# Kernel optimization log

Measured on AMD Instinct MI355X. Metric: run time of the kernel, lower is better.

Reference implementation:

```python
import jax, jax.numpy as jnp
import numpy as np

NUM_CLASSES = 20  # support_labels drawn from [0, 20); torch.unique over 200 samples yields all 20 w.h.p.


def setup_inputs() -> dict:
    key = jax.random.key(0)
    k1, k2, k3 = jax.random.split(key, 3)
    support_features = jax.random.normal(k1, (8, 200, 512), dtype=jnp.float32)
    support_labels = jax.random.randint(k2, (200,), 0, NUM_CLASSES, dtype=jnp.int64)
    query_features = jax.random.normal(k3, (8, 1024, 512), dtype=jnp.float32)
    return {
        "support_features": support_features,
        "support_labels": support_labels,
        "query_features": query_features,
    }


def _task_cov(x):
    # x: (P, T, F) -> per-phi covariance over the T samples, factor 1/(T-1)
    T = x.shape[1]
    xc = x - jnp.mean(x, axis=1, keepdims=True)
    return jnp.einsum("ptf,ptg->pfg", xc, xc) / (T - 1)


def reference(support_features, support_labels, query_features):
    P, T, F = support_features.shape
    C = NUM_CLASSES

    onehot = jax.nn.one_hot(support_labels, C, dtype=support_features.dtype)  # (T, C)
    counts = onehot.sum(axis=0)                                               # (C,)
    counts_safe = jnp.maximum(counts, 1.0)

    # per-class means: (P, C, F)
    class_means = jnp.einsum("ptf,tc->pcf", support_features, onehot) / counts_safe[None, :, None]

    # per-class covariance with 1/(n_c - 1) factor (matches _estimate_cov after transpose)
    centered = support_features[:, :, None, :] - class_means[:, None, :, :]   # (P, T, C, F)
    masked = centered * onehot[None, :, :, None]                               # zero out other classes
    denom = jnp.maximum(counts - 1.0, 1.0)
    class_cov = jnp.einsum("ptcf,ptcg->pcfg", masked, masked) / denom[None, :, None, None]

    task_cov = _task_cov(support_features)                                     # (P, F, F)

    lam = counts_safe / (counts_safe + 1.0)                                    # (C,)
    eye = jnp.eye(F, dtype=support_features.dtype)
    cov_reg = (lam[None, :, None, None] * class_cov
               + (1.0 - lam)[None, :, None, None] * task_cov[:, None]
               + eye)                                                          # (P, C, F, F)
    precision = jnp.linalg.inv(cov_reg)                                        # (P, C, F, F)

    # Mahalanobis quadratic form: diff^T P diff for every (phi, query, class)
    diff = class_means[:, None, :, :] - query_features[:, :, None, :]          # (P, Q, C, F)
    quad = jnp.einsum("pqcf,pcfg,pqcg->pqc", diff, precision, diff)
    mean_logits = (-quad).mean(axis=0)                                         # (Q, C)
    return mean_logits, class_means
```

## Files before the change

kernel.cpp:

```cpp
#include <hip/hip_runtime.h>

#define P 8
#define T 200
#define C 20
#define F 512
#define NQ 1024
#define MAXN 40
#define MMAX (T + MAXN)
#define PACK ((MMAX*(MMAX+1))/2)
#define PACKA 29280
#define PACKT 40960
#define QL (NQ*C)
#define NB 16
#define NTF 512
#define ETH 72
#define XQS 72

#define NBLK_FACTOR 160
#define NBLK_SQ     128
#define NBLK_MEANS  160
#define NBLK_QNORM  128
#define NBLK_TOTAL  (NBLK_FACTOR + NBLK_SQ + NBLK_MEANS + NBLK_QNORM)

enum : int {
  OFF_G    = 0,
  OFF_SQ   = OFF_G   + P*T*T,
  OFF_G1   = OFF_SQ  + P*T*NQ,
  OFF_GG   = OFF_G1  + P*T,
  OFF_GM   = OFF_GG  + P,
  OFF_GMC  = OFF_GM  + P*T*C,
  OFF_MM   = OFF_GMC + P*C,
  OFF_GQ   = OFF_MM  + P*C,
  OFF_QN   = OFF_GQ  + P*NQ,
  OFF_MQ   = OFF_QN  + P*NQ,
  OFF_W    = OFF_MQ  + P*C*NQ,
  OFF_QUAD = OFF_W   + P*C*PACKT,
  OFF_CLSF = OFF_QUAD+ P*NQ*C,
  OFF_INT  = OFF_CLSF+ C*8
};

typedef _Float16 f16x8 __attribute__((ext_vector_type(8)));
typedef _Float16 f16x4 __attribute__((ext_vector_type(4)));
typedef _Float16 f16x2 __attribute__((ext_vector_type(2)));
typedef float    f32x4 __attribute__((ext_vector_type(4)));

__device__ __forceinline__ int offr(int i){ return (i*(i+1))>>1; }

__device__ __forceinline__ int rowS(int i){
  int a = i >> 2, r = i & 3;
  return 8*a*(a+1) + 4*r*(a+1);
}

__device__ __forceinline__ int rowT(int r){
  const int R = r >> 6, s = r & 63;
  const int base = 4096 * ((R*(R+1)) >> 1);
  return base + s*((R+1) << 6);
}

__device__ __forceinline__ int row_of(int e){
  int i = (int)((sqrtf(8.f*(float)e + 1.f) - 1.f) * 0.5f);
  while (offr(i+1) <= e) ++i;
  while (offr(i) > e) --i;
  return i;
}

__device__ __forceinline__ int row_ofS(int e){
  int i = (int)sqrtf(2.f*(float)e);
  if (i > MMAX-1) i = MMAX-1;
  while (i < MMAX-1 && rowS(i+1) <= e) ++i;
  while (i > 0 && rowS(i) > e) --i;
  return i;
}

__global__ void k_setup(const int* lab, float* ws){
  int c = threadIdx.x;
  if (c >= C) return;
  int* wsI = (int*)(ws + OFF_INT);
  int n = 0;
  for (int t = 0; t < T; ++t){
    if (lab[t] == c){ if (n < MAXN) wsI[C + c*MAXN + n] = t; ++n; }
  }
  if (n > MAXN) n = MAXN;
  wsI[c] = n;
  float nf    = (float)n;
  float nsafe = fmaxf(nf, 1.0f);
  float dn    = fmaxf(nf - 1.0f, 1.0f);
  float lam   = nsafe / (nsafe + 1.0f);
  float sv    = (1.0f - lam) / (float)(T - 1);
  float av    = lam / dn;
  float* cf = ws + OFF_CLSF + c*8;
  cf[0] = nsafe; cf[1] = dn; cf[2] = lam; cf[3] = sv; cf[4] = av;
  cf[5] = sqrtf(sv); cf[6] = sqrtf(av); cf[7] = 0.0f;
}

__global__ __launch_bounds__(256) void k_gram(const float* X, float* ws){
  __shared__ float Xi[32][33];
  __shared__ float Xj[32][33];
  const int p = blockIdx.z, i0 = blockIdx.y*32, j0 = blockIdx.x*32;
  const int tx = threadIdx.x, ty = threadIdx.y;
  const int tid = ty*16 + tx;
  const float* Xp = X + (size_t)p*T*F;
  float acc[2][2] = {{0.f,0.f},{0.f,0.f}};
  for (int kb = 0; kb < F; kb += 32){
    for (int e = tid; e < 32*32; e += 256){
      int r = e >> 5, kk = e & 31;
      Xi[r][kk] = (i0+r < T) ? Xp[(i0+r)*F + kb+kk] : 0.f;
      Xj[r][kk] = (j0+r < T) ? Xp[(j0+r)*F + kb+kk] : 0.f;
    }
    __syncthreads();
    for (int kk = 0; kk < 32; ++kk){
      float a0 = Xi[2*ty][kk],   a1 = Xi[2*ty+1][kk];
      float b0 = Xj[2*tx][kk],   b1 = Xj[2*tx+1][kk];
      acc[0][0] += a0*b0; acc[0][1] += a0*b1;
      acc[1][0] += a1*b0; acc[1][1] += a1*b1;
    }
    __syncthreads();
  }
  float* Gp = ws + OFF_G + (size_t)p*T*T;
  for (int a = 0; a < 2; ++a)
    for (int b = 0; b < 2; ++b){
      int i = i0 + 2*ty + a, j = j0 + 2*tx + b;
      if (i < T && j < T) Gp[i*T + j] = acc[a][b];
    }
}

__global__ __launch_bounds__(256) void k_pstats_a(float* ws){
  const int p = blockIdx.y, bx = blockIdx.x;
  const int w = threadIdx.x >> 6, lane = threadIdx.x & 63;
  const int* wsI = (const int*)(ws + OFF_INT);
  const float* Gp = ws + OFF_G + (size_t)p*T*T;
  float* g1 = ws + OFF_G1 + p*T;
  float* Gm = ws + OFF_GM + (size_t)p*T*C;
  for (int rr = 0; rr < 2; ++rr){
    const int t = bx*8 + w*2 + rr;
    float s = 0.f;
    for (int u = lane; u < T; u += 64) s += Gp[t*T + u];
    for (int off = 32; off; off >>= 1) s += __shfl_down(s, off, 64);
    if (lane == 0) g1[t] = s * (1.0f/T);
    if (lane < C){
      int c = lane, nn = wsI[c];
      const int* idxc = wsI + C + c*MAXN;
      float sc = 0.f;
      for (int j = 0; j < nn; ++j) sc += Gp[t*T + idxc[j]];
      Gm[t*C + c] = sc / ws[OFF_CLSF + c*8];
    }
  }
}

__global__ __launch_bounds__(256) void k_pstats_b(float* ws){
  __shared__ float red[64];
  const int p = blockIdx.x, tid = threadIdx.x;
  const int* wsI = (const int*)(ws + OFF_INT);
  const float* g1 = ws + OFF_G1 + p*T;
  const float* Gm = ws + OFF_GM + (size_t)p*T*C;
  if (tid < 64){
    float s = 0.f;
    for (int t = tid; t < T; t += 64) s += g1[t];
    red[tid] = s;
  }
  __syncthreads();
  if (tid == 0){
    float s = 0.f;
    for (int k = 0; k < 64; ++k) s += red[k];
    ws[OFF_GG + p] = s * (1.0f/T);
  }
  if (tid < C){
    int c = tid, nn = wsI[c];
    const int* idxc = wsI + C + c*MAXN;
    float s = 0.f;
    for (int t = 0; t < T; ++t) s += Gm[t*C + c];
    ws[OFF_GMC + p*C + c] = s * (1.0f/T);
    float s2 = 0.f;
    for (int j = 0; j < nn; ++j) s2 += Gm[idxc[j]*C + c];
    ws[OFF_MM + p*C + c] = s2 / ws[OFF_CLSF + c*8];
  }
}

__global__ __launch_bounds__(256) void k_qstats(float* ws){
  __shared__ float red[4][64];
  const int p = blockIdx.y;
  const int qb = blockIdx.x*64;
  const int chunk = threadIdx.x >> 6, lane = threadIdx.x & 63;
  const int q = qb + lane;
  const int* wsI = (const int*)(ws + OFF_INT);
  const float* SQp = ws + OFF_SQ + (size_t)p*T*NQ;
  float s = 0.f;
  for (int t = chunk*50; t < chunk*50 + 50; ++t) s += SQp[t*NQ + q];
  red[chunk][lane] = s;
  __syncthreads();
  if (chunk == 0){
    float tot = red[0][lane] + red[1][lane] + red[2][lane] + red[3][lane];
    ws[OFF_GQ + p*NQ + q] = tot * (1.0f/T);
  }
  for (int c = chunk; c < C; c += 4){
    int nn = wsI[c];
    const int* idxc = wsI + C + c*MAXN;
    float sc = 0.f;
    for (int j = 0; j < nn; ++j) sc += SQp[idxc[j]*NQ + q];
    ws[OFF_MQ + ((size_t)(p*C + c))*NQ + q] = sc / ws[OFF_CLSF + c*8];
  }
}


union __align__(16) BigShared {
  struct { float Lp[PACKA]; float Sb[16*228]; float Dv[NB][NB+1]; } f;
  struct { _Float16 XHs[64*XQS], XLs[64*XQS], QHs[256*XQS], QLs[256*XQS]; } q;
};

__global__ __launch_bounds__(NTF) void k_big(const float* __restrict__ X,
                                             const float* __restrict__ Qf,
                                             float* __restrict__ ws,
                                             float* __restrict__ out){
  __shared__ BigShared u;
  const int bid = blockIdx.x;
  const int tid = threadIdx.x;
  const int* wsI = (const int*)(ws + OFF_INT);

  if (bid < NBLK_FACTOR){
    float* Lp = u.f.Lp;
    float* Sb = u.f.Sb;
    float (&Dv)[NB][NB+1] = u.f.Dv;
    const int blk = bid, p = blk / C, c = blk % C;
    const int n = wsI[c];
    const int m = T + n;
    const int* idxc = wsI + C + c*MAXN;
    const float* cf = ws + OFF_CLSF + c*8;
    const float sv = cf[3], av = cf[4], sqsa = cf[5]*cf[6];
    const float* Gp  = ws + OFF_G  + (size_t)p*T*T;
    const float* g1p = ws + OFF_G1 + p*T;
    const float  ggv = ws[OFF_GG + p];
    const float* Gmp = ws + OFF_GM + (size_t)p*T*C;
    const float gmcv = ws[OFF_GMC + p*C + c];
    const float mmv  = ws[OFF_MM  + p*C + c];

    for (int e = tid; e < PACKA; e += NTF){
      int i = row_ofS(e);
      int j = e - rowS(i);
      float v = 0.f;
      if (i < m && j <= i){
        if (i < T){
          v = sv*(Gp[i*T + j] - g1p[i] - g1p[j] + ggv);
          if (j == i) v += 1.0f;
        } else {
          int ua = idxc[i - T];
          if (j < T){
            v = sqsa*(Gp[ua*T + j] - Gmp[j*C + c] - g1p[ua] + gmcv);
          } else {
            int ub = idxc[j - T];
            v = av*(Gp[ua*T + ub] - Gmp[ua*C + c] - Gmp[ub*C + c] + mmv);
            if (j == i) v += 1.0f;
          }
        }
      }
      Lp[e] = v;
    }
    __syncthreads();

    for (int k0 = 0; k0 < m; k0 += NB){
      if (tid < 64){
        const int lane = tid;
        float a[NB];
        #pragma unroll
        for (int j = 0; j < NB; ++j){
          a[j] = 0.f;
          if (lane < NB && j <= lane) a[j] = Lp[rowS(k0+lane) + k0 + j];
        }
        #pragma unroll
        for (int k = 0; k < NB; ++k){
          float akk = __shfl(a[k], k, 64);
          float inv = rsqrtf(akk);
          a[k] *= inv;
          #pragma unroll
          for (int j = k+1; j < NB; ++j){
            float ljk = __shfl(a[k], j, 64);
            a[j] -= a[k] * ljk;
          }
        }
        float x[NB];
        #pragma unroll
        for (int i = 0; i < NB; ++i){
          float Lii = __shfl(a[i], i, 64);
          float sxx = 0.f;
          #pragma unroll
          for (int k2 = 0; k2 < i; ++k2){
            float Lik = __shfl(a[k2], i, 64);
            sxx += Lik * x[k2];
          }
          float tt = ((i == lane) ? 1.f : 0.f) - sxx;
          x[i] = tt / Lii;
        }
        if (lane < NB){
          #pragma unroll
          for (int i = 0; i < NB; ++i){
            Dv[i][lane] = (i >= lane) ? x[i] : 0.f;
            if (i >= lane) Lp[rowS(k0+i) + k0 + lane] = x[i];
          }
        }
      }
      __syncthreads();

      for (int r = k0 + NB + tid; r < m; r += NTF){
        const int o = rowS(r) + k0;
        float4 A0 = *(const float4*)&Lp[o];
        float4 A1 = *(const float4*)&Lp[o+4];
        float4 A2 = *(const float4*)&Lp[o+8];
        float4 A3 = *(const float4*)&Lp[o+12];
        float ar[NB] = {A0.x,A0.y,A0.z,A0.w, A1.x,A1.y,A1.z,A1.w,
                        A2.x,A2.y,A2.z,A2.w, A3.x,A3.y,A3.z,A3.w};
        float sr[NB];
        #pragma unroll
        for (int j = 0; j < NB; ++j){
          float s = 0.f;
          #pragma unroll
          for (int kk = 0; kk <= j; ++kk) s += ar[kk] * Dv[j][kk];
          sr[j] = s;
        }
        *(float4*)&Lp[o]    = make_float4(sr[0], sr[1], sr[2], sr[3]);
        *(float4*)&Lp[o+4]  = make_float4(sr[4], sr[5], sr[6], sr[7]);
        *(float4*)&Lp[o+8]  = make_float4(sr[8], sr[9], sr[10], sr[11]);
        *(float4*)&Lp[o+12] = make_float4(sr[12], sr[13], sr[14], sr[15]);
      }
      __syncthreads();

      const int rs = m - k0 - NB;
      if (rs > 0){
        const int base = k0 + NB;
        const int nt4 = (rs + 3) >> 2;
        const int ntile = (nt4*(nt4+1)) >> 1;
        for (int e2 = tid; e2 < ntile; e2 += NTF){
          const int ti = row_of(e2);
          const int tj = e2 - offr(ti);
          const int gi0 = base + 4*ti, gj0 = base + 4*tj;
          const float* pa0 = &Lp[rowS(gi0)   + k0];
          const float* pa1 = &Lp[rowS(gi0+1) + k0];
          const float* pa2 = &Lp[rowS(gi0+2) + k0];
          const float* pa3 = &Lp[rowS(gi0+3) + k0];
          const float* pb0 = &Lp[rowS(gj0)   + k0];
          const float* pb1 = &Lp[rowS(gj0+1) + k0];
          const float* pb2 = &Lp[rowS(gj0+2) + k0];
          const float* pb3 = &Lp[rowS(gj0+3) + k0];
          float acc[4][4] = {};
          #pragma unroll
          for (int kk = 0; kk < NB; kk += 4){
            float4 a0 = *(const float4*)(pa0+kk);
            float4 a1 = *(const float4*)(pa1+kk);
            float4 a2 = *(const float4*)(pa2+kk);
            float4 a3 = *(const float4*)(pa3+kk);
            float4 b0 = *(const float4*)(pb0+kk);
            float4 b1 = *(const float4*)(pb1+kk);
            float4 b2 = *(const float4*)(pb2+kk);
            float4 b3 = *(const float4*)(pb3+kk);
            acc[0][0] += a0.x*b0.x + a0.y*b0.y + a0.z*b0.z + a0.w*b0.w;
            acc[0][1] += a0.x*b1.x + a0.y*b1.y + a0.z*b1.z + a0.w*b1.w;
            acc[0][2] += a0.x*b2.x + a0.y*b2.y + a0.z*b2.z + a0.w*b2.w;
            acc[0][3] += a0.x*b3.x + a0.y*b3.y + a0.z*b3.z + a0.w*b3.w;
            acc[1][0] += a1.x*b0.x + a1.y*b0.y + a1.z*b0.z + a1.w*b0.w;
            acc[1][1] += a1.x*b1.x + a1.y*b1.y + a1.z*b1.z + a1.w*b1.w;
            acc[1][2] += a1.x*b2.x + a1.y*b2.y + a1.z*b2.z + a1.w*b2.w;
            acc[1][3] += a1.x*b3.x + a1.y*b3.y + a1.z*b3.z + a1.w*b3.w;
            acc[2][0] += a2.x*b0.x + a2.y*b0.y + a2.z*b0.z + a2.w*b0.w;
            acc[2][1] += a2.x*b1.x + a2.y*b1.y + a2.z*b1.z + a2.w*b1.w;
            acc[2][2] += a2.x*b2.x + a2.y*b2.y + a2.z*b2.z + a2.w*b2.w;
            acc[2][3] += a2.x*b3.x + a2.y*b3.y + a2.z*b3.z + a2.w*b3.w;
            acc[3][0] += a3.x*b0.x + a3.y*b0.y + a3.z*b0.z + a3.w*b0.w;
            acc[3][1] += a3.x*b1.x + a3.y*b1.y + a3.z*b1.z + a3.w*b1.w;
            acc[3][2] += a3.x*b2.x + a3.y*b2.y + a3.z*b2.z + a3.w*b2.w;
            acc[3][3] += a3.x*b3.x + a3.y*b3.y + a3.z*b3.z + a3.w*b3.w;
          }
          #pragma unroll
          for (int u2 = 0; u2 < 4; ++u2){
            const int gi = gi0 + u2;
            if (gi < m){
              const int og = rowS(gi);
              if (gj0 + 3 <= gi){
                float4 t = *(float4*)&Lp[og + gj0];
                t.x -= acc[u2][0]; t.y -= acc[u2][1]; t.z -= acc[u2][2]; t.w -= acc[u2][3];
                *(float4*)&Lp[og + gj0] = t;
              } else {
                #pragma unroll
                for (int v = 0; v < 4; ++v){
                  const int gj = gj0 + v;
                  if (gj <= gi) Lp[og + gj] -= acc[u2][v];
                }
              }
            }
          }
        }
      }
      __syncthreads();
    }

    for (int I = 1; I < MMAX/NB; ++I){
      const int i0 = I*NB;
      const int nct = i0 >> 2;
      const int rt = tid & 3, ct = tid >> 2;
      const int rt4 = rt*4;
      const int j0 = ct*4;
      int o0 = 0, o1 = 0, o2 = 0, o3 = 0;
      if (tid < 4*nct){
        const int r0 = i0 + rt4;
        o0 = rowS(r0); o1 = rowS(r0+1); o2 = rowS(r0+2); o3 = rowS(r0+3);
        float acc[4][4] = {};
        for (int k = j0; k < i0; k += 4){
          float4 l0 = *(const float4*)&Lp[o0+k];
          float4 l1 = *(const float4*)&Lp[o1+k];
          float4 l2 = *(const float4*)&Lp[o2+k];
          float4 l3 = *(const float4*)&Lp[o3+k];
          float4 x0 = *(const float4*)&Lp[rowS(k)  +j0];
          float4 x1 = *(const float4*)&Lp[rowS(k+1)+j0];
          float4 x2 = *(const float4*)&Lp[rowS(k+2)+j0];
          float4 x3 = *(const float4*)&Lp[rowS(k+3)+j0];
          acc[0][0] += l0.x*x0.x + l0.y*x1.x + l0.z*x2.x + l0.w*x3.x;
          acc[0][1] += l0.x*x0.y + l0.y*x1.y + l0.z*x2.y + l0.w*x3.y;
          acc[0][2] += l0.x*x0.z + l0.y*x1.z + l0.z*x2.z + l0.w*x3.z;
          acc[0][3] += l0.x*x0.w + l0.y*x1.w + l0.z*x2.w + l0.w*x3.w;
          acc[1][0] += l1.x*x0.x + l1.y*x1.x + l1.z*x2.x + l1.w*x3.x;
          acc[1][1] += l1.x*x0.y + l1.y*x1.y + l1.z*x2.y + l1.w*x3.y;
          acc[1][2] += l1.x*x0.z + l1.y*x1.z + l1.z*x2.z + l1.w*x3.z;
          acc[1][3] += l1.x*x0.w + l1.y*x1.w + l1.z*x2.w + l1.w*x3.w;
          acc[2][0] += l2.x*x0.x + l2.y*x1.x + l2.z*x2.x + l2.w*x3.x;
          acc[2][1] += l2.x*x0.y + l2.y*x1.y + l2.z*x2.y + l2.w*x3.y;
          acc[2][2] += l2.x*x0.z + l2.y*x1.z + l2.z*x2.z + l2.w*x3.z;
          acc[2][3] += l2.x*x0.w + l2.y*x1.w + l2.z*x2.w + l2.w*x3.w;
          acc[3][0] += l3.x*x0.x + l3.y*x1.x + l3.z*x2.x + l3.w*x3.x;
          acc[3][1] += l3.x*x0.y + l3.y*x1.y + l3.z*x2.y + l3.w*x3.y;
          acc[3][2] += l3.x*x0.z + l3.y*x1.z + l3.z*x2.z + l3.w*x3.z;
          acc[3][3] += l3.x*x0.w + l3.y*x1.w + l3.z*x2.w + l3.w*x3.w;
        }
        *(float4*)&Sb[(rt4  )*228 + j0] = make_float4(acc[0][0], acc[0][1], acc[0][2], acc[0][3]);
        *(float4*)&Sb[(rt4+1)*228 + j0] = make_float4(acc[1][0], acc[1][1], acc[1][2], acc[1][3]);
        *(float4*)&Sb[(rt4+2)*228 + j0] = make_float4(acc[2][0], acc[2][1], acc[2][2], acc[2][3]);
        *(float4*)&Sb[(rt4+3)*228 + j0] = make_float4(acc[3][0], acc[3][1], acc[3][2], acc[3][3]);
      }
      __syncthreads();
      if (tid < 4*nct){
        float acc[4][4] = {};
        for (int s = 0; s < rt4 + 4; ++s){
          const float d0 = Lp[o0 + i0 + s];
          const float d1 = Lp[o1 + i0 + s];
          const float d2 = Lp[o2 + i0 + s];
          const float d3 = Lp[o3 + i0 + s];
          const float4 sv4 = *(const float4*)&Sb[s*228 + j0];
          acc[0][0] += d0*sv4.x; acc[0][1] += d0*sv4.y; acc[0][2] += d0*sv4.z; acc[0][3] += d0*sv4.w;
          acc[1][0] += d1*sv4.x; acc[1][1] += d1*sv4.y; acc[1][2] += d1*sv4.z; acc[1][3] += d1*sv4.w;
          acc[2][0] += d2*sv4.x; acc[2][1] += d2*sv4.y; acc[2][2] += d2*sv4.z; acc[2][3] += d2*sv4.w;
          acc[3][0] += d3*sv4.x; acc[3][1] += d3*sv4.y; acc[3][2] += d3*sv4.z; acc[3][3] += d3*sv4.w;
        }
        *(float4*)&Lp[o0 + j0] = make_float4(-acc[0][0], -acc[0][1], -acc[0][2], -acc[0][3]);
        *(float4*)&Lp[o1 + j0] = make_float4(-acc[1][0], -acc[1][1], -acc[1][2], -acc[1][3]);
        *(float4*)&Lp[o2 + j0] = make_float4(-acc[2][0], -acc[2][1], -acc[2][2], -acc[2][3]);
        *(float4*)&Lp[o3 + j0] = make_float4(-acc[3][0], -acc[3][1], -acc[3][2], -acc[3][3]);
      }
      __syncthreads();
    }

    _Float16* WH = (_Float16*)(ws + OFF_W) + (size_t)blk * (2*PACKT);
    _Float16* WL = WH + PACKT;
    for (int e = tid; e < 64*64; e += NTF){
      int s = e >> 6, j = e & 63, r = s;
      float v = (r < m && j <= r) ? Lp[rowS(r) + j] : 0.f;
      _Float16 h = (_Float16)v;
      WH[e] = h; WL[e] = (_Float16)(v - (float)h);
    }
    for (int e = tid; e < 64*128; e += NTF){
      int s = e >> 7, j = e & 127, r = 64 + s;
      float v = (r < m && j <= r) ? Lp[rowS(r) + j] : 0.f;
      _Float16 h = (_Float16)v;
      WH[4096 + e] = h; WL[4096 + e] = (_Float16)(v - (float)h);
    }
    for (int e = tid; e < 64*192; e += NTF){
      int x = e >> 6;
      int s = (x*171) >> 9;
      int j = e - s*192, r = 128 + s;
      float v = (r < m && j <= r) ? Lp[rowS(r) + j] : 0.f;
      _Float16 h = (_Float16)v;
      WH[12288 + e] = h; WL[12288 + e] = (_Float16)(v - (float)h);
    }
    for (int e = tid; e < 64*256; e += NTF){
      int s = e >> 8, j = e & 255, r = 192 + s;
      float v = (r < m && j <= r) ? Lp[rowS(r) + j] : 0.f;
      _Float16 h = (_Float16)v;
      WH[24576 + e] = h; WL[24576 + e] = (_Float16)(v - (float)h);
    }

  } else if (bid < NBLK_FACTOR + NBLK_SQ){
    const int sb = bid - NBLK_FACTOR;
    const int p = sb >> 4, rem = sb & 15;
    const int t0 = (rem >> 2) * 64;
    const int qb = (rem & 3) * 256;
    _Float16* XH = u.q.XHs; _Float16* XL = u.q.XLs;
    _Float16* QH = u.q.QHs; _Float16* Qlo = u.q.QLs;
    const float* Xp = X  + (size_t)p*T*F;
    const float* Qp = Qf + (size_t)p*NQ*F;
    const int wv = tid >> 6, ln = tid & 63;
    const int lr = ln & 15, lg = ln >> 4;
    const int wt = (wv & 1) * 32;
    const int wq = (wv >> 1) * 64;

    f32x4 acc[2][4] = {};

    for (int kb = 0; kb < F; kb += 64){
      for (int e = tid; e < 64*16; e += NTF){
        const int r = e >> 4, l4 = (e & 15) * 4;
        float4 v = (t0 + r < T) ? *(const float4*)&Xp[(size_t)(t0+r)*F + kb + l4]
                                : make_float4(0.f,0.f,0.f,0.f);
        _Float16 h0=(_Float16)v.x, h1=(_Float16)v.y, h2=(_Float16)v.z, h3=(_Float16)v.w;
        f16x4 hv = {h0,h1,h2,h3};
        f16x4 lv = {(_Float16)(v.x-(float)h0),(_Float16)(v.y-(float)h1),
                    (_Float16)(v.z-(float)h2),(_Float16)(v.w-(float)h3)};
        *(f16x4*)&XH[r*XQS + l4] = hv;
        *(f16x4*)&XL[r*XQS + l4] = lv;
      }
      for (int e = tid; e < 256*16; e += NTF){
        const int r = e >> 4, l4 = (e & 15) * 4;
        float4 v = *(const float4*)&Qp[(size_t)(qb+r)*F + kb + l4];
        _Float16 h0=(_Float16)v.x, h1=(_Float16)v.y, h2=(_Float16)v.z, h3=(_Float16)v.w;
        f16x4 hv = {h0,h1,h2,h3};
        f16x4 lv = {(_Float16)(v.x-(float)h0),(_Float16)(v.y-(float)h1),
                    (_Float16)(v.z-(float)h2),(_Float16)(v.w-(float)h3)};
        *(f16x4*)&QH[r*XQS + l4] = hv;
        *(f16x4*)&Qlo[r*XQS + l4] = lv;
      }
      __syncthreads();
      #pragma unroll
      for (int s = 0; s < 2; ++s){
        const int ko = s*32 + 8*lg;
        f16x8 bh[4], bl[4];
        #pragma unroll
        for (int j = 0; j < 4; ++j){
          const int qr = wq + j*16 + lr;
          bh[j] = *(const f16x8*)&QH[qr*XQS + ko];
          bl[j] = *(const f16x8*)&Qlo[qr*XQS + ko];
        }
        #pragma unroll
        for (int i = 0; i < 2; ++i){
          const int tr = wt + i*16 + lr;
          f16x8 ah = *(const f16x8*)&XH[tr*XQS + ko];
          f16x8 al = *(const f16x8*)&XL[tr*XQS + ko];
          #pragma unroll
          for (int j = 0; j < 4; ++j){
            acc[i][j] = __builtin_amdgcn_mfma_f32_16x16x32_f16(ah, bh[j], acc[i][j], 0, 0, 0);
            acc[i][j] = __builtin_amdgcn_mfma_f32_16x16x32_f16(ah, bl[j], acc[i][j], 0, 0, 0);
            acc[i][j] = __builtin_amdgcn_mfma_f32_16x16x32_f16(al, bh[j], acc[i][j], 0, 0, 0);
          }
        }
      }
      __syncthreads();
    }
    float* SQp = ws + OFF_SQ + (size_t)p*T*NQ;
    #pragma unroll
    for (int i = 0; i < 2; ++i){
      const int tb = t0 + wt + i*16 + lg*4;
      #pragma unroll
      for (int j = 0; j < 4; ++j){
        const int qc = qb + wq + j*16 + lr;
        #pragma unroll
        for (int r = 0; r < 4; ++r){
          const int t = tb + r;
          if (t < T) SQp[t*NQ + qc] = acc[i][j][r];
        }
      }
    }

  } else if (bid < NBLK_FACTOR + NBLK_SQ + NBLK_MEANS){
    const int mb = bid - NBLK_FACTOR - NBLK_SQ;
    const int p = mb / C, c = mb % C;
    const int n = wsI[c];
    const int* idxc = wsI + C + c*MAXN;
    const float nf = ws[OFF_CLSF + c*8];
    const float* Xp = X + (size_t)p*T*F;
    float* o = out + QL + (size_t)(p*C + c)*F;
    for (int f = tid; f < F; f += NTF){
      float s = 0.f;
      for (int j = 0; j < n; ++j) s += Xp[idxc[j]*F + f];
      o[f] = s / nf;
    }

  } else {
    const int qb2 = bid - NBLK_FACTOR - NBLK_SQ - NBLK_MEANS;
    const int w = tid >> 6, lane = tid & 63;
    const int row0 = qb2*64 + w*8;
    for (int i = 0; i < 8; ++i){
      const int row = row0 + i;
      const float4* q4p = (const float4*)(Qf + (size_t)row*F);
      float4 v0 = q4p[lane];
      float4 v1 = q4p[lane + 64];
      float s = v0.x*v0.x + v0.y*v0.y + v0.z*v0.z + v0.w*v0.w
              + v1.x*v1.x + v1.y*v1.y + v1.z*v1.z + v1.w*v1.w;
      for (int off = 32; off; off >>= 1) s += __shfl_down(s, off, 64);
      if (lane == 0) ws[OFF_QN + row] = s;
    }
  }
}

__global__ __launch_bounds__(256) void k_apply(float* ws){
  __shared__ __align__(16) _Float16 EtH[64*ETH];
  __shared__ __align__(16) _Float16 EtL[64*ETH];
  __shared__ float Ef[32*65];
  __shared__ float Part[4][64];
  const int p = blockIdx.z, c = blockIdx.y, q0 = blockIdx.x*64;
  const int tid = threadIdx.x;
  const int* wsI = (const int*)(ws + OFF_INT);
  const int n = wsI[c], m = T + n;
  const int* idxc = wsI + C + c*MAXN;
  const float* cf = ws + OFF_CLSF + c*8;
  const float sqs = cf[5], sqa = cf[6];
  const float gmcv = ws[OFF_GMC + p*C + c];
  const float mmv  = ws[OFF_MM  + p*C + c];
  const float* Gmp = ws + OFF_GM + (size_t)p*T*C;
  const float* SQp = ws + OFF_SQ + (size_t)p*T*NQ;
  const float* gqp = ws + OFF_GQ + p*NQ + q0;
  const float* qnp = ws + OFF_QN + p*NQ + q0;
  const float* mqp = ws + OFF_MQ + ((size_t)(p*C + c))*NQ + q0;

  const int wv = tid >> 6, ln = tid & 63;
  const int lr = ln & 15;
  const int lg = ln >> 4;
  const _Float16* WH = (const _Float16*)(ws + OFF_W) + (size_t)(p*C + c)*(2*PACKT);
  const _Float16* WL = WH + PACKT;
  int aoff[4];
  #pragma unroll
  for (int i = 0; i < 4; ++i){
    const int t = wv + 4*i;
    aoff[i] = rowT(16*t + lr) + 8*lg;
  }

  f32x4 acc[4][4] = {};

  for (int h = 0; h < 4; ++h){
    for (int ch = 0; ch < 2; ++ch){
      const int jbl = ch*32;
      const int jb = h*64 + jbl;
      for (int e = tid; e < 32*64; e += 256){
        const int jl = e >> 6, q = e & 63;
        const int j = jb + jl;
        float v = 0.f;
        if (j < T){
          v = sqs*(Gmp[j*C + c] - SQp[j*NQ + q0 + q] - gmcv + gqp[q]);
        } else if (j < m){
          const int u2 = idxc[j - T];
          v = sqa*(Gmp[u2*C + c] - SQp[u2*NQ + q0 + q] - mmv + mqp[q]);
        }
        Ef[jl*65 + q] = v;
      }
      __syncthreads();
      for (int e = tid; e < 16*64; e += 256){
        const int jp = e & 15, q = e >> 4;
        const int jl = 2*jp;
        const float v0 = Ef[jl*65 + q];
        const float v1 = Ef[(jl+1)*65 + q];
        const _Float16 h0 = (_Float16)v0, h1 = (_Float16)v1;
        f16x2 hv; hv[0] = h0; hv[1] = h1;
        f16x2 lv; lv[0] = (_Float16)(v0 - (float)h0); lv[1] = (_Float16)(v1 - (float)h1);
        *(f16x2*)&EtH[q*ETH + jbl + jl] = hv;
        *(f16x2*)&EtL[q*ETH + jbl + jl] = lv;
      }
      __syncthreads();
    }

    #pragma unroll
    for (int sl = 0; sl < 2; ++sl){
      const int s = 2*h + sl;
      if (2*s > wv + 12) continue;
      const int k0 = 32*s;
      const int bo = lr*ETH + (k0 - 64*h) + 8*lg;
      f16x8 bh[4], bl[4];
      #pragma unroll
      for (int ct2 = 0; ct2 < 4; ++ct2){
        bh[ct2] = *(const f16x8*)&EtH[ct2*16*ETH + bo];
        bl[ct2] = *(const f16x8*)&EtL[ct2*16*ETH + bo];
      }
      #pragma unroll
      for (int i = 0; i < 4; ++i){
        const int t = wv + 4*i;
        if (2*s <= t){
          f16x8 ah = *(const f16x8*)(WH + aoff[i] + k0);
          f16x8 al = *(const f16x8*)(WL + aoff[i] + k0);
          #pragma unroll
          for (int ct2 = 0; ct2 < 4; ++ct2){
            acc[i][ct2] = __builtin_amdgcn_mfma_f32_16x16x32_f16(ah, bh[ct2], acc[i][ct2], 0, 0, 0);
            acc[i][ct2] = __builtin_amdgcn_mfma_f32_16x16x32_f16(ah, bl[ct2], acc[i][ct2], 0, 0, 0);
            acc[i][ct2] = __builtin_amdgcn_mfma_f32_16x16x32_f16(al, bh[ct2], acc[i][ct2], 0, 0, 0);
          }
        }
      }
    }
  }

  #pragma unroll
  for (int ct2 = 0; ct2 < 4; ++ct2){
    float sthread = 0.f;
    #pragma unroll
    for (int i = 0; i < 4; ++i){
      const f32x4 a4 = acc[i][ct2];
      sthread += a4[0]*a4[0] + a4[1]*a4[1] + a4[2]*a4[2] + a4[3]*a4[3];
    }
    sthread += __shfl_xor(sthread, 16, 64);
    sthread += __shfl_xor(sthread, 32, 64);
    if (ln < 16) Part[wv][ct2*16 + ln] = sthread;
  }
  __syncthreads();
  if (tid < 64){
    const float tt = Part[0][tid] + Part[1][tid] + Part[2][tid] + Part[3][tid];
    const float quad = mmv - 2.f*mqp[tid] + qnp[tid] - tt;
    ws[OFF_QUAD + ((size_t)p*NQ + q0 + tid)*C + c] = quad;
  }
}

__global__ void k_logits(const float* ws, float* out){
  int lin = blockIdx.x*256 + threadIdx.x;
  if (lin < QL){
    float s = 0.f;
    for (int p = 0; p < P; ++p) s += ws[OFF_QUAD + (size_t)p*NQ*C + lin];
    out[lin] = -s * (1.0f/P);
  }
}

extern "C" void kernel_launch(void* const* d_in, const int* in_sizes, int n_in,
                              void* d_out, int out_size, void* d_ws, size_t ws_size,
                              hipStream_t stream){
  const float* X   = (const float*)d_in[0];
  const int*   lab = (const int*)d_in[1];
  const float* Qf  = (const float*)d_in[2];
  float* out = (float*)d_out;
  float* ws  = (float*)d_ws;

  k_setup   <<<1, 64, 0, stream>>>(lab, ws);
  k_gram    <<<dim3(7,7,P),  dim3(16,16), 0, stream>>>(X, ws);
  k_pstats_a<<<dim3(25,P), 256, 0, stream>>>(ws);
  k_pstats_b<<<P, 256, 0, stream>>>(ws);
  k_big     <<<NBLK_TOTAL, NTF, 0, stream>>>(X, Qf, ws, out);
  k_qstats  <<<dim3(16,P), 256, 0, stream>>>(ws);
  k_apply   <<<dim3(16,C,P), 256, 0, stream>>>(ws);
  k_logits  <<<QL/256, 256, 0, stream>>>(ws, out);
}
```

Baseline: 565.6 us.

## Build split-f16 E tile directly in registers and skip empty Cholesky blocks

In k_apply, each thread now computes 16 consecutive j values for one query in registers, splits them into high and low f16 parts, and writes them to the EtH/EtL shared tiles with vector stores. This removes the intermediate fp32 Ef staging buffer, one transpose pass, and two barriers per half-chunk. Separately, the blocked factorization loop exits once the block row passes the active size m, skipping trailing blocks beyond the class's augmented dimension. The trade-off is more registers per thread in k_apply.

```diff
diff --git a/kernel.cpp b/kernel.cpp
--- a/kernel.cpp
+++ b/kernel.cpp
@@ -392,6 +392,7 @@
 
     for (int I = 1; I < MMAX/NB; ++I){
       const int i0 = I*NB;
+      if (i0 >= m) break;
       const int nct = i0 >> 2;
       const int rt = tid & 3, ct = tid >> 2;
       const int rt4 = rt*4;
@@ -596,7 +597,6 @@
 __global__ __launch_bounds__(256) void k_apply(float* ws){
   __shared__ __align__(16) _Float16 EtH[64*ETH];
   __shared__ __align__(16) _Float16 EtL[64*ETH];
-  __shared__ float Ef[32*65];
   __shared__ float Part[4][64];
   const int p = blockIdx.z, c = blockIdx.y, q0 = blockIdx.x*64;
   const int tid = threadIdx.x;
@@ -625,38 +625,47 @@
     aoff[i] = rowT(16*t + lr) + 8*lg;
   }
 
+  const int bq = tid & 63;
+  const int jg = tid >> 6;
+  const float gqv = gqp[bq];
+  const float mqv = mqp[bq];
+
   f32x4 acc[4][4] = {};
 
   for (int h = 0; h < 4; ++h){
-    for (int ch = 0; ch < 2; ++ch){
-      const int jbl = ch*32;
-      const int jb = h*64 + jbl;
-      for (int e = tid; e < 32*64; e += 256){
-        const int jl = e >> 6, q = e & 63;
-        const int j = jb + jl;
+    if (h) __syncthreads();
+    {
+      const int jb = h*64 + jg*16;
+      float vv[16];
+      #pragma unroll
+      for (int uu = 0; uu < 16; ++uu){
+        const int j = jb + uu;
         float v = 0.f;
         if (j < T){
-          v = sqs*(Gmp[j*C + c] - SQp[j*NQ + q0 + q] - gmcv + gqp[q]);
+          v = sqs*(Gmp[j*C + c] - SQp[j*NQ + q0 + bq] - gmcv + gqv);
         } else if (j < m){
           const int u2 = idxc[j - T];
-          v = sqa*(Gmp[u2*C + c] - SQp[u2*NQ + q0 + q] - mmv + mqp[q]);
-        }
-        Ef[jl*65 + q] = v;
-      }
-      __syncthreads();
-      for (int e = tid; e < 16*64; e += 256){
-        const int jp = e & 15, q = e >> 4;
-        const int jl = 2*jp;
-        const float v0 = Ef[jl*65 + q];
-        const float v1 = Ef[(jl+1)*65 + q];
-        const _Float16 h0 = (_Float16)v0, h1 = (_Float16)v1;
-        f16x2 hv; hv[0] = h0; hv[1] = h1;
-        f16x2 lv; lv[0] = (_Float16)(v0 - (float)h0); lv[1] = (_Float16)(v1 - (float)h1);
-        *(f16x2*)&EtH[q*ETH + jbl + jl] = hv;
-        *(f16x2*)&EtL[q*ETH + jbl + jl] = lv;
-      }
-      __syncthreads();
-    }
+          v = sqa*(Gmp[u2*C + c] - SQp[u2*NQ + q0 + bq] - mmv + mqv);
+        }
+        vv[uu] = v;
+      }
+      f16x8 hv0, hv1, lv0, lv1;
+      #pragma unroll
+      for (int uu = 0; uu < 8; ++uu){
+        const _Float16 ha = (_Float16)vv[uu];
+        const _Float16 hb = (_Float16)vv[8+uu];
+        hv0[uu] = ha; hv1[uu] = hb;
+        lv0[uu] = (_Float16)(vv[uu]   - (float)ha);
+        lv1[uu] = (_Float16)(vv[8+uu] - (float)hb);
+      }
+      _Float16* dh = &EtH[bq*ETH + jg*16];
+      _Float16* dl = &EtL[bq*ETH + jg*16];
+      *(f16x8*)dh       = hv0;
+      *(f16x8*)(dh + 8) = hv1;
+      *(f16x8*)dl       = lv0;
+      *(f16x8*)(dl + 8) = lv1;
+    }
+    __syncthreads();
 
     #pragma unroll
     for (int sl = 0; sl < 2; ++sl){
```

New measurement: 574.9 us. No clear change (+1.7%).

## Compute support Gram matrix with split-fp16 MFMA and skip empty Cholesky blocks

Applied to the files above, without the earlier changes.

Rewrites the Gram kernel so each 512-thread block computes a 64-row by 256-column slab using fp16 MFMA instructions. Each fp32 value is split into high and low fp16 halves, and three products are summed to approximate fp32 accuracy. This replaces the scalar FMA tiling with matrix-core throughput. It also adds an early exit in the blocked factorization loop once the block index passes the active size m, which skips panels of zero work. The split-fp16 scheme drops the low×low term, so it can lose a little precision.

```diff
diff --git a/kernel.cpp b/kernel.cpp
--- a/kernel.cpp
+++ b/kernel.cpp
@@ -93,35 +93,85 @@
   cf[5] = sqrtf(sv); cf[6] = sqrtf(av); cf[7] = 0.0f;
 }
 
-__global__ __launch_bounds__(256) void k_gram(const float* X, float* ws){
-  __shared__ float Xi[32][33];
-  __shared__ float Xj[32][33];
-  const int p = blockIdx.z, i0 = blockIdx.y*32, j0 = blockIdx.x*32;
-  const int tx = threadIdx.x, ty = threadIdx.y;
-  const int tid = ty*16 + tx;
+__global__ __launch_bounds__(512) void k_gram(const float* __restrict__ X,
+                                              float* __restrict__ ws){
+  __shared__ _Float16 RH[64*XQS], RL[64*XQS];
+  __shared__ _Float16 CH[256*XQS], CL[256*XQS];
+  const int p = blockIdx.y, t0 = blockIdx.x*64;
+  const int tid = threadIdx.x;
   const float* Xp = X + (size_t)p*T*F;
-  float acc[2][2] = {{0.f,0.f},{0.f,0.f}};
-  for (int kb = 0; kb < F; kb += 32){
-    for (int e = tid; e < 32*32; e += 256){
-      int r = e >> 5, kk = e & 31;
-      Xi[r][kk] = (i0+r < T) ? Xp[(i0+r)*F + kb+kk] : 0.f;
-      Xj[r][kk] = (j0+r < T) ? Xp[(j0+r)*F + kb+kk] : 0.f;
+  const int wv = tid >> 6, ln = tid & 63;
+  const int lr = ln & 15, lg = ln >> 4;
+  const int wt = (wv & 1) * 32;
+  const int wq = (wv >> 1) * 64;
+
+  f32x4 acc[2][4] = {};
+
+  for (int kb = 0; kb < F; kb += 64){
+    for (int e = tid; e < 64*16; e += 512){
+      const int r = e >> 4, l4 = (e & 15) * 4;
+      float4 v = (t0 + r < T) ? *(const float4*)&Xp[(size_t)(t0+r)*F + kb + l4]
+                              : make_float4(0.f,0.f,0.f,0.f);
+      _Float16 h0=(_Float16)v.x, h1=(_Float16)v.y, h2=(_Float16)v.z, h3=(_Float16)v.w;
+      f16x4 hv = {h0,h1,h2,h3};
+      f16x4 lv = {(_Float16)(v.x-(float)h0),(_Float16)(v.y-(float)h1),
+                  (_Float16)(v.z-(float)h2),(_Float16)(v.w-(float)h3)};
+      *(f16x4*)&RH[r*XQS + l4] = hv;
+      *(f16x4*)&RL[r*XQS + l4] = lv;
+    }
+    for (int e = tid; e < 256*16; e += 512){
+      const int r = e >> 4, l4 = (e & 15) * 4;
+      float4 v = (r < T) ? *(const float4*)&Xp[(size_t)r*F + kb + l4]
+                         : make_float4(0.f,0.f,0.f,0.f);
+      _Float16 h0=(_Float16)v.x, h1=(_Float16)v.y, h2=(_Float16)v.z, h3=(_Float16)v.w;
+      f16x4 hv = {h0,h1,h2,h3};
+      f16x4 lv = {(_Float16)(v.x-(float)h0),(_Float16)(v.y-(float)h1),
+                  (_Float16)(v.z-(float)h2),(_Float16)(v.w-(float)h3)};
+      *(f16x4*)&CH[r*XQS + l4] = hv;
+      *(f16x4*)&CL[r*XQS + l4] = lv;
     }
     __syncthreads();
-    for (int kk = 0; kk < 32; ++kk){
-      float a0 = Xi[2*ty][kk],   a1 = Xi[2*ty+1][kk];
-      float b0 = Xj[2*tx][kk],   b1 = Xj[2*tx+1][kk];
-      acc[0][0] += a0*b0; acc[0][1] += a0*b1;
-      acc[1][0] += a1*b0; acc[1][1] += a1*b1;
+    #pragma unroll
+    for (int s = 0; s < 2; ++s){
+      const int ko = s*32 + 8*lg;
+      f16x8 bh[4], bl[4];
+      #pragma unroll
+      for (int j = 0; j < 4; ++j){
+        const int qr = wq + j*16 + lr;
+        bh[j] = *(const f16x8*)&CH[qr*XQS + ko];
+        bl[j] = *(const f16x8*)&CL[qr*XQS + ko];
+      }
+      #pragma unroll
+      for (int i = 0; i < 2; ++i){
+        const int tr = wt + i*16 + lr;
+        f16x8 ah = *(const f16x8*)&RH[tr*XQS + ko];
+        f16x8 al = *(const f16x8*)&RL[tr*XQS + ko];
+        #pragma unroll
+        for (int j = 0; j < 4; ++j){
+          acc[i][j] = __builtin_amdgcn_mfma_f32_16x16x32_f16(ah, bh[j], acc[i][j], 0, 0, 0);
+          acc[i][j] = __builtin_amdgcn_mfma_f32_16x16x32_f16(ah, bl[j], acc[i][j], 0, 0, 0);
+          acc[i][j] = __builtin_amdgcn_mfma_f32_16x16x32_f16(al, bh[j], acc[i][j], 0, 0, 0);
+        }
+      }
     }
     __syncthreads();
   }
   float* Gp = ws + OFF_G + (size_t)p*T*T;
-  for (int a = 0; a < 2; ++a)
-    for (int b = 0; b < 2; ++b){
-      int i = i0 + 2*ty + a, j = j0 + 2*tx + b;
-      if (i < T && j < T) Gp[i*T + j] = acc[a][b];
-    }
+  #pragma unroll
+  for (int i = 0; i < 2; ++i){
+    const int tb = t0 + wt + i*16 + lg*4;
+    #pragma unroll
+    for (int j = 0; j < 4; ++j){
+      const int col = wq + j*16 + lr;
+      if (col < T){
+        #pragma unroll
+        for (int r = 0; r < 4; ++r){
+          const int t = tb + r;
+          if (t < T) Gp[t*T + col] = acc[i][j][r];
+        }
+      }
+    }
+  }
 }
 
 __global__ __launch_bounds__(256) void k_pstats_a(float* ws){
@@ -392,6 +442,7 @@
 
     for (int I = 1; I < MMAX/NB; ++I){
       const int i0 = I*NB;
+      if (i0 >= m) break;
       const int nct = i0 >> 2;
       const int rt = tid & 3, ct = tid >> 2;
       const int rt4 = rt*4;
@@ -726,7 +777,7 @@
   float* ws  = (float*)d_ws;
 
   k_setup   <<<1, 64, 0, stream>>>(lab, ws);
-  k_gram    <<<dim3(7,7,P),  dim3(16,16), 0, stream>>>(X, ws);
+  k_gram    <<<dim3(4,P), 512, 0, stream>>>(X, ws);
   k_pstats_a<<<dim3(25,P), 256, 0, stream>>>(ws);
   k_pstats_b<<<P, 256, 0, stream>>>(ws);
   k_big     <<<NBLK_TOTAL, NTF, 0, stream>>>(X, Qf, ws, out);
```

After: 538.3 us (median of 2 runs). -4.8%, faster.
